# Optimization experiments

Hardware: AMD Instinct MI355X
Metric: run time of the kernel (lower is better)

## Reference

```python
import jax, jax.numpy as jnp
import numpy as np

B, S, I, H, L, O = 64, 512, 128, 1024, 3, 128


def _gru_cell(x, h, Wx, Wh, bh):
    # Wx: [3, H, in], Wh: [3, H, H], bh: [3, H]; gate order (z, r, g).
    # Matches: z = sig(W_xz x + W_hz h + b_z); r = sig(W_xr x + W_hr h + b_r);
    #          g = tanh(W_xg x + W_hg (r*h) + b_g); h' = z*h + (1-z)*g
    z = jax.nn.sigmoid(x @ Wx[0].T + h @ Wh[0].T + bh[0])
    r = jax.nn.sigmoid(x @ Wx[1].T + h @ Wh[1].T + bh[1])
    g = jnp.tanh(x @ Wx[2].T + (r * h) @ Wh[2].T + bh[2])
    return z * h + (1.0 - z) * g


def setup_inputs() -> dict:
    key = jax.random.key(0)
    ks = jax.random.split(key, 10)
    u = lambda k, shape, fan: jax.random.uniform(k, shape, jnp.float32, -1.0, 1.0) / np.float32(np.sqrt(fan))
    return {
        "x": jax.random.normal(ks[0], (B, S, I), jnp.float32),
        # layer 0 (input dim I)
        "Wx0": u(ks[1], (3, H, I), I),
        "Wh0": u(ks[2], (3, H, H), H),
        "bh0": u(ks[3], (3, H), H),
        # layers 1..L-1 (input dim H), stacked on leading axis
        "Wxr": u(ks[4], (L - 1, 3, H, H), H),
        "Whr": u(ks[5], (L - 1, 3, H, H), H),
        "bhr": u(ks[6], (L - 1, 3, H), H),
        # output projection
        "Wout": u(ks[7], (O, H), H),
        "bout": u(ks[8], (O,), H),
    }


def reference(x, Wx0, Wh0, bh0, Wxr, Whr, bhr, Wout, bout):
    batch = x.shape[0]
    n_rest = Wxr.shape[0]
    h_init = jnp.zeros((n_rest + 1, batch, H), x.dtype)  # [L, B, H]

    def step(hs, x_t):
        new = []
        h = _gru_cell(x_t, hs[0], Wx0, Wh0, bh0)
        new.append(h)
        inp = h
        for j in range(n_rest):  # small fixed layer count
            h = _gru_cell(inp, hs[j + 1], Wxr[j], Whr[j], bhr[j])
            new.append(h)
            inp = h
        y = inp @ Wout.T + bout
        return jnp.stack(new), y

    hs_final, ys = jax.lax.scan(step, h_init, jnp.swapaxes(x, 0, 1))
    layer_output = jnp.swapaxes(ys, 0, 1)        # (B, S, O)
    hidden_state = jnp.swapaxes(hs_final, 0, 1)  # (B, L, H)
    return layer_output, hidden_state
```

## Files before the change

### kernel.cpp

```cpp
#include <hip/hip_runtime.h>


namespace {
constexpr int kB = 64, kS = 512, kI = 128, kH = 1024, kO = 128;
constexpr int kTicks = kS + 3;
constexpr size_t kBSO = (size_t)kB * kS * kO;
constexpr int kTasksA = 792, kTasksB = 384;

__device__ float g_wxt0[3 * 128 * 1024];
__device__ float g_wht0[3 * 1024 * 1024];
__device__ float g_wxtr[6 * 1024 * 1024];
__device__ float g_whtr[6 * 1024 * 1024];
__device__ float g_woutT[1024 * 128];
__device__ float g_xT[512 * 128 * 64];
__device__ float g_hbuf[2 * 3 * 1024 * 64];
__device__ float g_zT[3 * 1024 * 64];
__device__ float g_rhT[3 * 1024 * 64];
__device__ float g_gxT[3 * 1024 * 64];
__device__ float g_partA[kTasksA * 4096];
__device__ float g_partB[kTasksB * 4096];
}


__global__ void zero_hbuf() {
  g_hbuf[blockIdx.x * 256 + threadIdx.x] = 0.f;
}

__global__ __launch_bounds__(256) void transpose_k(
    const float* __restrict__ in, int sel, int R, int C) {
  float* out;
  switch (sel) {
    case 0: out = g_wxt0; break;
    case 1: out = g_wht0; break;
    case 2: out = g_wxtr; break;
    case 3: out = g_whtr; break;
    case 4: out = g_woutT; break;
    default: out = g_xT; break;
  }
  const size_t mat = (size_t)R * C;
  in += blockIdx.z * mat;
  out += blockIdx.z * mat;
  __shared__ float t[32][33];
  const int c0 = blockIdx.x * 32, r0 = blockIdx.y * 32;
  const int tx = threadIdx.x & 31, ty = threadIdx.x >> 5;
  for (int i = ty; i < 32; i += 8) {
    const int r = r0 + i, c = c0 + tx;
    if (r < R && c < C) t[i][tx] = in[(size_t)r * C + c];
  }
  __syncthreads();
  for (int i = ty; i < 32; i += 8) {
    const int c = c0 + i, r = r0 + tx;
    if (c < C && r < R) out[(size_t)c * R + r] = t[tx][i];
  }
}

__device__ __forceinline__ void load_lds16(const float* g, float* l) {
  __builtin_amdgcn_global_load_lds(
      (const __attribute__((address_space(1))) void*)g,
      (__attribute__((address_space(3))) void*)l, 16, 0, 0);
}

__global__ __launch_bounds__(256, 2) void gemm_tasks(int phase, int tau) {
  const int id = blockIdx.x;
  const int par = tau & 1;
  const float* hb = g_hbuf + par * 196608;

  int l = 0, t_l = 0;
  const float* inp = nullptr; const float* w = nullptr;
  const float* inp2 = nullptr; const float* w2 = nullptr;
  int nk = 0, nk2 = 0, ldw = 1024;

  if (phase == 0) {
    if (id < 128) {
      const int gate = id >> 6, rem = id & 63;
      const int tile = rem >> 2, ks = rem & 3, n0 = tile * 64;
      t_l = tau;
      const float* wh = g_wht0 + (size_t)gate * 1048576;
      if (ks == 0) {
        inp = g_xT + (size_t)t_l * 8192; nk = 128;
        w = g_wxt0 + (size_t)gate * 131072 + n0;
        inp2 = hb; nk2 = 256; w2 = wh + n0;
      } else {
        const int k0 = ks * 256;
        inp = hb + k0 * 64; nk = 256;
        w = wh + (size_t)k0 * 1024 + n0;
      }
    } else if (id < 640) {
      const int q = id - 128;
      l = 1 + (q >> 8);
      const int qq = q & 255, gate = qq >> 7, rem = qq & 127;
      const int tile = rem >> 3, ks = rem & 7, n0 = tile * 64;
      t_l = tau - l;
      if (ks < 4) {
        const int k0 = ks * 256;
        inp = hb + (l - 1) * 65536 + k0 * 64; nk = 256;
        w = g_wxtr + (size_t)((l - 1) * 3 + gate) * 1048576 + (size_t)k0 * 1024 + n0;
      } else {
        const int k0 = (ks - 4) * 256;
        inp = hb + l * 65536 + k0 * 64; nk = 256;
        w = g_whtr + (size_t)((l - 1) * 3 + gate) * 1048576 + (size_t)k0 * 1024 + n0;
      }
    } else if (id < 656) {
      const int tile = id - 640;
      t_l = tau;
      inp = g_xT + (size_t)t_l * 8192; nk = 128;
      w = g_wxt0 + (size_t)2 * 131072 + tile * 64;
    } else if (id < 784) {
      const int q = id - 656;
      l = 1 + (q >> 6);
      const int qq = q & 63, tile = qq >> 2, ks = qq & 3;
      t_l = tau - l;
      const int k0 = ks * 256;
      inp = hb + (l - 1) * 65536 + k0 * 64; nk = 256;
      w = g_wxtr + (size_t)((l - 1) * 3 + 2) * 1048576 + (size_t)k0 * 1024 + tile * 64;
    } else {
      const int q = id - 784, tile = q >> 2, ks = q & 3;
      t_l = tau - 3;
      const int k0 = ks * 256;
      inp = hb + 2 * 65536 + k0 * 64; nk = 256;
      w = g_woutT + (size_t)k0 * 128 + tile * 64; ldw = 128;
    }
  } else {
    l = id >> 7;
    const int rem = id & 127, tile = rem >> 3, ks = rem & 7;
    t_l = tau - l;
    const int k0 = ks * 128;
    inp = g_rhT + l * 65536 + k0 * 64; nk = 128;
    w = ((l == 0) ? g_wht0 + (size_t)2 * 1048576
                  : g_whtr + (size_t)((l - 1) * 3 + 2) * 1048576) +
        (size_t)k0 * 1024 + tile * 64;
  }
  if (t_l < 0 || t_l >= kS) return;

  __shared__ float sI[64 * 64];
  __shared__ float sW[64 * 64];
  const int tid = threadIdx.x;
  const int tn = (tid & 15) * 4, tb = (tid >> 4) * 4;
  float acc[4][4] = {};

  for (int seg = 0; seg < 2; ++seg) {
    const float* ip; const float* wp; int kn;
    if (seg == 0) { ip = inp; wp = w; kn = nk; }
    else { if (!nk2) break; ip = inp2; wp = w2; kn = nk2; }
    for (int c0 = 0; c0 < kn; c0 += 64) {
#pragma unroll
      for (int u = 0; u < 4; ++u) {
        const int idx = tid + u * 256;
        load_lds16(ip + c0 * 64 + idx * 4, sI + idx * 4);
      }
#pragma unroll
      for (int u = 0; u < 4; ++u) {
        const int idx = tid + u * 256, k = idx >> 4, f = idx & 15;
        load_lds16(wp + (size_t)(c0 + k) * ldw + f * 4, sW + idx * 4);
      }
      __syncthreads();
#pragma unroll 8
      for (int k = 0; k < 64; ++k) {
        const float4 a = *(const float4*)(sI + k * 64 + tb);
        const float4 wv = *(const float4*)(sW + k * 64 + tn);
        acc[0][0] += wv.x * a.x; acc[0][1] += wv.x * a.y; acc[0][2] += wv.x * a.z; acc[0][3] += wv.x * a.w;
        acc[1][0] += wv.y * a.x; acc[1][1] += wv.y * a.y; acc[1][2] += wv.y * a.z; acc[1][3] += wv.y * a.w;
        acc[2][0] += wv.z * a.x; acc[2][1] += wv.z * a.y; acc[2][2] += wv.z * a.z; acc[2][3] += wv.z * a.w;
        acc[3][0] += wv.w * a.x; acc[3][1] += wv.w * a.y; acc[3][2] += wv.w * a.z; acc[3][3] += wv.w * a.w;
      }
      __syncthreads();
    }
  }

  float* po = ((phase == 0) ? g_partA : g_partB) + (size_t)id * 4096;
#pragma unroll
  for (int i = 0; i < 4; ++i) {
    float4 v = {acc[i][0], acc[i][1], acc[i][2], acc[i][3]};
    *(float4*)(po + (tn + i) * 64 + tb) = v;
  }
}

__global__ __launch_bounds__(256) void reduceA(
    int tau, const float* __restrict__ Bh0, const float* __restrict__ Bhr,
    const float* __restrict__ Bout, float* __restrict__ Out) {
  const int gid = blockIdx.x * 256 + threadIdx.x;
  const int b0 = (gid & 15) * 4, c = gid >> 4;
  const int par = tau & 1;
  if (c < 6144) {
    const int gate = (c >= 3072) ? 1 : 0;
    const int cc = c - gate * 3072;
    const int l = cc >> 10, n = cc & 1023;
    const int t_l = tau - l;
    if (t_l < 0 || t_l >= kS) return;
    const int tile = n >> 6, cl = n & 63;
    int base, nks;
    if (l == 0)      { base = gate * 64 + tile * 4;        nks = 4; }
    else if (l == 1) { base = 128 + gate * 128 + tile * 8; nks = 8; }
    else             { base = 384 + gate * 128 + tile * 8; nks = 8; }
    const float bias = (l == 0) ? Bh0[gate * 1024 + n] : Bhr[(l - 1) * 3072 + gate * 1024 + n];
    float s0 = bias, s1 = bias, s2 = bias, s3 = bias;
    for (int j = 0; j < nks; ++j) {
      const float4 p = *(const float4*)&g_partA[(size_t)(base + j) * 4096 + cl * 64 + b0];
      s0 += p.x; s1 += p.y; s2 += p.z; s3 += p.w;
    }
    const float v0 = 1.f / (1.f + expf(-s0)), v1 = 1.f / (1.f + expf(-s1));
    const float v2 = 1.f / (1.f + expf(-s2)), v3 = 1.f / (1.f + expf(-s3));
    const int off = l * 65536 + n * 64 + b0;
    if (gate == 0) {
      *(float4*)&g_zT[off] = make_float4(v0, v1, v2, v3);
    } else {
      const float4 h = *(const float4*)&g_hbuf[par * 196608 + off];
      *(float4*)&g_rhT[off] = make_float4(v0 * h.x, v1 * h.y, v2 * h.z, v3 * h.w);
    }
  } else if (c < 9216) {
    const int cc = c - 6144, l = cc >> 10, n = cc & 1023;
    const int t_l = tau - l;
    if (t_l < 0 || t_l >= kS) return;
    const int tile = n >> 6, cl = n & 63;
    int base, nks;
    if (l == 0)      { base = 640 + tile;     nks = 1; }
    else if (l == 1) { base = 656 + tile * 4; nks = 4; }
    else             { base = 720 + tile * 4; nks = 4; }
    const float bias = (l == 0) ? Bh0[2048 + n] : Bhr[(l - 1) * 3072 + 2048 + n];
    float s0 = bias, s1 = bias, s2 = bias, s3 = bias;
    for (int j = 0; j < nks; ++j) {
      const float4 p = *(const float4*)&g_partA[(size_t)(base + j) * 4096 + cl * 64 + b0];
      s0 += p.x; s1 += p.y; s2 += p.z; s3 += p.w;
    }
    *(float4*)&g_gxT[l * 65536 + n * 64 + b0] = make_float4(s0, s1, s2, s3);
  } else {
    const int o = c - 9216, ty = tau - 3;
    if (ty < 0 || ty >= kS) return;
    const int tile = o >> 6, cl = o & 63, base = 784 + tile * 4;
    const float bias = Bout[o];
    float s0 = bias, s1 = bias, s2 = bias, s3 = bias;
    for (int j = 0; j < 4; ++j) {
      const float4 p = *(const float4*)&g_partA[(size_t)(base + j) * 4096 + cl * 64 + b0];
      s0 += p.x; s1 += p.y; s2 += p.z; s3 += p.w;
    }
    Out[((size_t)(b0 + 0) * kS + ty) * kO + o] = s0;
    Out[((size_t)(b0 + 1) * kS + ty) * kO + o] = s1;
    Out[((size_t)(b0 + 2) * kS + ty) * kO + o] = s2;
    Out[((size_t)(b0 + 3) * kS + ty) * kO + o] = s3;
  }
}

__global__ __launch_bounds__(256) void reduceB(
    int tau, float* __restrict__ Out) {
  const int gid = blockIdx.x * 256 + threadIdx.x;
  const int b0 = (gid & 15) * 4, c = gid >> 4;
  const int l = c >> 10, n = c & 1023;
  const int t_l = tau - l;
  if (t_l < 0 || t_l >= kS) return;
  const int par = tau & 1;
  const int tile = n >> 6, cl = n & 63;
  const int base = (l * 16 + tile) * 8;
  const int off = l * 65536 + n * 64 + b0;
  float4 gs = *(const float4*)&g_gxT[off];
  for (int j = 0; j < 8; ++j) {
    const float4 p = *(const float4*)&g_partB[(size_t)(base + j) * 4096 + cl * 64 + b0];
    gs.x += p.x; gs.y += p.y; gs.z += p.z; gs.w += p.w;
  }
  const float g0 = tanhf(gs.x), g1 = tanhf(gs.y), g2 = tanhf(gs.z), g3 = tanhf(gs.w);
  const float4 z = *(const float4*)&g_zT[off];
  const float4 h = *(const float4*)&g_hbuf[par * 196608 + off];
  float4 hn;
  hn.x = z.x * h.x + (1.f - z.x) * g0;
  hn.y = z.y * h.y + (1.f - z.y) * g1;
  hn.z = z.z * h.z + (1.f - z.z) * g2;
  hn.w = z.w * h.w + (1.f - z.w) * g3;
  *(float4*)&g_hbuf[(1 - par) * 196608 + off] = hn;
  if (t_l == kS - 1) {
    Out[kBSO + ((size_t)(b0 + 0) * 3 + l) * 1024 + n] = hn.x;
    Out[kBSO + ((size_t)(b0 + 1) * 3 + l) * 1024 + n] = hn.y;
    Out[kBSO + ((size_t)(b0 + 2) * 3 + l) * 1024 + n] = hn.z;
    Out[kBSO + ((size_t)(b0 + 3) * 3 + l) * 1024 + n] = hn.w;
  }
}

extern "C" void kernel_launch(void* const* d_in, const int* in_sizes, int n_in,
                              void* d_out, int out_size, void* d_ws, size_t ws_size,
                              hipStream_t stream) {
  const float* X    = (const float*)d_in[0];
  const float* Wx0  = (const float*)d_in[1];
  const float* Wh0  = (const float*)d_in[2];
  const float* bh0  = (const float*)d_in[3];
  const float* Wxr  = (const float*)d_in[4];
  const float* Whr  = (const float*)d_in[5];
  const float* bhr  = (const float*)d_in[6];
  const float* Wout = (const float*)d_in[7];
  const float* bout = (const float*)d_in[8];
  (void)d_ws; (void)ws_size;

  if (n_in != 9 ||
      in_sizes[0] != 64 * 512 * 128 || in_sizes[1] != 3 * 1024 * 128 ||
      in_sizes[2] != 3 * 1024 * 1024 || in_sizes[3] != 3 * 1024 ||
      in_sizes[4] != 2 * 3 * 1024 * 1024 || in_sizes[5] != 2 * 3 * 1024 * 1024 ||
      in_sizes[6] != 2 * 3 * 1024 || in_sizes[7] != 128 * 1024 ||
      in_sizes[8] != 128 || out_size != 64 * 512 * 128 + 64 * 3 * 1024)
    return;

  float* out = (float*)d_out;

  hipLaunchKernelGGL(zero_hbuf, dim3(1536), dim3(256), 0, stream);
  hipLaunchKernelGGL(transpose_k, dim3(4, 32, 3),   dim3(256), 0, stream, Wx0,  0, 1024, 128);
  hipLaunchKernelGGL(transpose_k, dim3(32, 32, 3),  dim3(256), 0, stream, Wh0,  1, 1024, 1024);
  hipLaunchKernelGGL(transpose_k, dim3(32, 32, 6),  dim3(256), 0, stream, Wxr,  2, 1024, 1024);
  hipLaunchKernelGGL(transpose_k, dim3(32, 32, 6),  dim3(256), 0, stream, Whr,  3, 1024, 1024);
  hipLaunchKernelGGL(transpose_k, dim3(32, 4, 1),   dim3(256), 0, stream, Wout, 4, 128, 1024);
  hipLaunchKernelGGL(transpose_k, dim3(2048, 2, 1), dim3(256), 0, stream, X,    5, 64, 65536);

  for (int tau = 0; tau < kTicks; ++tau) {
    hipLaunchKernelGGL(gemm_tasks, dim3(kTasksA), dim3(256), 0, stream, 0, tau);
    hipLaunchKernelGGL(reduceA, dim3(584), dim3(256), 0, stream,
                       tau, bh0, bhr, bout, out);
    if (tau < kTicks - 1) {
      hipLaunchKernelGGL(gemm_tasks, dim3(kTasksB), dim3(256), 0, stream, 1, tau);
      hipLaunchKernelGGL(reduceB, dim3(192), dim3(256), 0, stream, tau, out);
    }
  }
}
```

Baseline: 26.47 ms.

## Widen GEMM task tiles to 128 columns with 512-thread blocks and deeper K splits

Each GEMM task now covers 128 output columns with 512-thread blocks and 512-deep K slices, where it used to cover 64 columns with 256-deep slices. This cuts the task counts (792→218, 384→96), the partial sums written and read by the reduce kernels, and repeated loads of the input activations. The x-projection and Wh segments for layer 0 are now split into separate tasks instead of being chained in one block. In exchange, far fewer blocks run on a GPU with many CUs (MI355X), and each block does longer serial K loops, so parallelism may drop.

Result: slower. 32.70 ms (+23.6%).

```diff
diff --git a/kernel.cpp b/kernel.cpp
--- a/kernel.cpp
+++ b/kernel.cpp
@@ -5,7 +5,7 @@
 constexpr int kB = 64, kS = 512, kI = 128, kH = 1024, kO = 128;
 constexpr int kTicks = kS + 3;
 constexpr size_t kBSO = (size_t)kB * kS * kO;
-constexpr int kTasksA = 792, kTasksB = 384;
+constexpr int kTasksA = 218, kTasksB = 96;
 
 __device__ float g_wxt0[3 * 128 * 1024];
 __device__ float g_wht0[3 * 1024 * 1024];
@@ -17,8 +17,8 @@
 __device__ float g_zT[3 * 1024 * 64];
 __device__ float g_rhT[3 * 1024 * 64];
 __device__ float g_gxT[3 * 1024 * 64];
-__device__ float g_partA[kTasksA * 4096];
-__device__ float g_partB[kTasksB * 4096];
+__device__ float g_partA[kTasksA * 8192];
+__device__ float g_partB[kTasksB * 8192];
 }
 
 
@@ -60,114 +60,100 @@
       (__attribute__((address_space(3))) void*)l, 16, 0, 0);
 }
 
-__global__ __launch_bounds__(256, 2) void gemm_tasks(int phase, int tau) {
+__global__ __launch_bounds__(512) void gemm_tasks(int phase, int tau) {
   const int id = blockIdx.x;
   const int par = tau & 1;
   const float* hb = g_hbuf + par * 196608;
 
-  int l = 0, t_l = 0;
+  int t_l = 0, nk = 512, ldw = 1024;
   const float* inp = nullptr; const float* w = nullptr;
-  const float* inp2 = nullptr; const float* w2 = nullptr;
-  int nk = 0, nk2 = 0, ldw = 1024;
 
   if (phase == 0) {
-    if (id < 128) {
-      const int gate = id >> 6, rem = id & 63;
-      const int tile = rem >> 2, ks = rem & 3, n0 = tile * 64;
+    if (id < 48) {
+      const int gate = id / 24, q = id % 24, ng = q / 3, ks = q % 3;
       t_l = tau;
-      const float* wh = g_wht0 + (size_t)gate * 1048576;
       if (ks == 0) {
         inp = g_xT + (size_t)t_l * 8192; nk = 128;
-        w = g_wxt0 + (size_t)gate * 131072 + n0;
-        inp2 = hb; nk2 = 256; w2 = wh + n0;
+        w = g_wxt0 + (size_t)gate * 131072 + ng * 128;
       } else {
-        const int k0 = ks * 256;
-        inp = hb + k0 * 64; nk = 256;
-        w = wh + (size_t)k0 * 1024 + n0;
+        const int k0 = (ks - 1) * 512;
+        inp = hb + k0 * 64;
+        w = g_wht0 + (size_t)gate * 1048576 + (size_t)k0 * 1024 + ng * 128;
       }
-    } else if (id < 640) {
-      const int q = id - 128;
-      l = 1 + (q >> 8);
-      const int qq = q & 255, gate = qq >> 7, rem = qq & 127;
-      const int tile = rem >> 3, ks = rem & 7, n0 = tile * 64;
+    } else if (id < 176) {
+      const int q = id - 48, l = 1 + (q >> 6);
+      const int q2 = q & 63, gate = q2 >> 5, q3 = q2 & 31, ng = q3 >> 2, ks = q3 & 3;
       t_l = tau - l;
-      if (ks < 4) {
-        const int k0 = ks * 256;
-        inp = hb + (l - 1) * 65536 + k0 * 64; nk = 256;
-        w = g_wxtr + (size_t)((l - 1) * 3 + gate) * 1048576 + (size_t)k0 * 1024 + n0;
+      if (ks < 2) {
+        const int k0 = ks * 512;
+        inp = hb + (l - 1) * 65536 + k0 * 64;
+        w = g_wxtr + (size_t)((l - 1) * 3 + gate) * 1048576 + (size_t)k0 * 1024 + ng * 128;
       } else {
-        const int k0 = (ks - 4) * 256;
-        inp = hb + l * 65536 + k0 * 64; nk = 256;
-        w = g_whtr + (size_t)((l - 1) * 3 + gate) * 1048576 + (size_t)k0 * 1024 + n0;
+        const int k0 = (ks - 2) * 512;
+        inp = hb + l * 65536 + k0 * 64;
+        w = g_whtr + (size_t)((l - 1) * 3 + gate) * 1048576 + (size_t)k0 * 1024 + ng * 128;
       }
-    } else if (id < 656) {
-      const int tile = id - 640;
+    } else if (id < 184) {
+      const int ng = id - 176;
       t_l = tau;
       inp = g_xT + (size_t)t_l * 8192; nk = 128;
-      w = g_wxt0 + (size_t)2 * 131072 + tile * 64;
-    } else if (id < 784) {
-      const int q = id - 656;
-      l = 1 + (q >> 6);
-      const int qq = q & 63, tile = qq >> 2, ks = qq & 3;
+      w = g_wxt0 + (size_t)2 * 131072 + ng * 128;
+    } else if (id < 216) {
+      const int q = id - 184, l = 1 + (q >> 4);
+      const int q2 = q & 15, ng = q2 >> 1, ks = q2 & 1;
       t_l = tau - l;
-      const int k0 = ks * 256;
-      inp = hb + (l - 1) * 65536 + k0 * 64; nk = 256;
-      w = g_wxtr + (size_t)((l - 1) * 3 + 2) * 1048576 + (size_t)k0 * 1024 + tile * 64;
+      const int k0 = ks * 512;
+      inp = hb + (l - 1) * 65536 + k0 * 64;
+      w = g_wxtr + (size_t)((l - 1) * 3 + 2) * 1048576 + (size_t)k0 * 1024 + ng * 128;
     } else {
-      const int q = id - 784, tile = q >> 2, ks = q & 3;
+      const int ks = id - 216;
       t_l = tau - 3;
-      const int k0 = ks * 256;
-      inp = hb + 2 * 65536 + k0 * 64; nk = 256;
-      w = g_woutT + (size_t)k0 * 128 + tile * 64; ldw = 128;
+      const int k0 = ks * 512;
+      inp = hb + 2 * 65536 + k0 * 64;
+      w = g_woutT + (size_t)k0 * 128; ldw = 128;
     }
   } else {
-    l = id >> 7;
-    const int rem = id & 127, tile = rem >> 3, ks = rem & 7;
+    const int l = id >> 5, q = id & 31, ng = q >> 2, ks = q & 3;
     t_l = tau - l;
-    const int k0 = ks * 128;
-    inp = g_rhT + l * 65536 + k0 * 64; nk = 128;
+    const int k0 = ks * 256;
+    inp = g_rhT + l * 65536 + k0 * 64; nk = 256;
     w = ((l == 0) ? g_wht0 + (size_t)2 * 1048576
                   : g_whtr + (size_t)((l - 1) * 3 + 2) * 1048576) +
-        (size_t)k0 * 1024 + tile * 64;
+        (size_t)k0 * 1024 + ng * 128;
   }
   if (t_l < 0 || t_l >= kS) return;
 
   __shared__ float sI[64 * 64];
-  __shared__ float sW[64 * 64];
+  __shared__ float sW[64 * 128];
   const int tid = threadIdx.x;
-  const int tn = (tid & 15) * 4, tb = (tid >> 4) * 4;
+  const int tn = (tid & 31) * 4, tb = (tid >> 5) * 4;
   float acc[4][4] = {};
 
-  for (int seg = 0; seg < 2; ++seg) {
-    const float* ip; const float* wp; int kn;
-    if (seg == 0) { ip = inp; wp = w; kn = nk; }
-    else { if (!nk2) break; ip = inp2; wp = w2; kn = nk2; }
-    for (int c0 = 0; c0 < kn; c0 += 64) {
+  for (int c0 = 0; c0 < nk; c0 += 64) {
 #pragma unroll
-      for (int u = 0; u < 4; ++u) {
-        const int idx = tid + u * 256;
-        load_lds16(ip + c0 * 64 + idx * 4, sI + idx * 4);
-      }
+    for (int u = 0; u < 2; ++u) {
+      const int idx = tid + u * 512;
+      load_lds16(inp + c0 * 64 + idx * 4, sI + idx * 4);
+    }
 #pragma unroll
-      for (int u = 0; u < 4; ++u) {
-        const int idx = tid + u * 256, k = idx >> 4, f = idx & 15;
-        load_lds16(wp + (size_t)(c0 + k) * ldw + f * 4, sW + idx * 4);
-      }
-      __syncthreads();
+    for (int u = 0; u < 4; ++u) {
+      const int idx = tid + u * 512, k = idx >> 5, f = idx & 31;
+      load_lds16(w + (size_t)(c0 + k) * ldw + f * 4, sW + idx * 4);
+    }
+    __syncthreads();
 #pragma unroll 8
-      for (int k = 0; k < 64; ++k) {
-        const float4 a = *(const float4*)(sI + k * 64 + tb);
-        const float4 wv = *(const float4*)(sW + k * 64 + tn);
-        acc[0][0] += wv.x * a.x; acc[0][1] += wv.x * a.y; acc[0][2] += wv.x * a.z; acc[0][3] += wv.x * a.w;
-        acc[1][0] += wv.y * a.x; acc[1][1] += wv.y * a.y; acc[1][2] += wv.y * a.z; acc[1][3] += wv.y * a.w;
-        acc[2][0] += wv.z * a.x; acc[2][1] += wv.z * a.y; acc[2][2] += wv.z * a.z; acc[2][3] += wv.z * a.w;
-        acc[3][0] += wv.w * a.x; acc[3][1] += wv.w * a.y; acc[3][2] += wv.w * a.z; acc[3][3] += wv.w * a.w;
-      }
-      __syncthreads();
-    }
-  }
-
-  float* po = ((phase == 0) ? g_partA : g_partB) + (size_t)id * 4096;
+    for (int k = 0; k < 64; ++k) {
+      const float4 a = *(const float4*)(sI + k * 64 + tb);
+      const float4 wv = *(const float4*)(sW + k * 128 + tn);
+      acc[0][0] += wv.x * a.x; acc[0][1] += wv.x * a.y; acc[0][2] += wv.x * a.z; acc[0][3] += wv.x * a.w;
+      acc[1][0] += wv.y * a.x; acc[1][1] += wv.y * a.y; acc[1][2] += wv.y * a.z; acc[1][3] += wv.y * a.w;
+      acc[2][0] += wv.z * a.x; acc[2][1] += wv.z * a.y; acc[2][2] += wv.z * a.z; acc[2][3] += wv.z * a.w;
+      acc[3][0] += wv.w * a.x; acc[3][1] += wv.w * a.y; acc[3][2] += wv.w * a.z; acc[3][3] += wv.w * a.w;
+    }
+    __syncthreads();
+  }
+
+  float* po = ((phase == 0) ? g_partA : g_partB) + (size_t)id * 8192;
 #pragma unroll
   for (int i = 0; i < 4; ++i) {
     float4 v = {acc[i][0], acc[i][1], acc[i][2], acc[i][3]};
@@ -187,15 +173,14 @@
     const int l = cc >> 10, n = cc & 1023;
     const int t_l = tau - l;
     if (t_l < 0 || t_l >= kS) return;
-    const int tile = n >> 6, cl = n & 63;
+    const int ng = n >> 7, cl = n & 127;
     int base, nks;
-    if (l == 0)      { base = gate * 64 + tile * 4;        nks = 4; }
-    else if (l == 1) { base = 128 + gate * 128 + tile * 8; nks = 8; }
-    else             { base = 384 + gate * 128 + tile * 8; nks = 8; }
+    if (l == 0) { base = gate * 24 + ng * 3;                  nks = 3; }
+    else        { base = 48 + (l - 1) * 64 + gate * 32 + ng * 4; nks = 4; }
     const float bias = (l == 0) ? Bh0[gate * 1024 + n] : Bhr[(l - 1) * 3072 + gate * 1024 + n];
     float s0 = bias, s1 = bias, s2 = bias, s3 = bias;
     for (int j = 0; j < nks; ++j) {
-      const float4 p = *(const float4*)&g_partA[(size_t)(base + j) * 4096 + cl * 64 + b0];
+      const float4 p = *(const float4*)&g_partA[(size_t)(base + j) * 8192 + cl * 64 + b0];
       s0 += p.x; s1 += p.y; s2 += p.z; s3 += p.w;
     }
     const float v0 = 1.f / (1.f + expf(-s0)), v1 = 1.f / (1.f + expf(-s1));
@@ -211,26 +196,24 @@
     const int cc = c - 6144, l = cc >> 10, n = cc & 1023;
     const int t_l = tau - l;
     if (t_l < 0 || t_l >= kS) return;
-    const int tile = n >> 6, cl = n & 63;
+    const int ng = n >> 7, cl = n & 127;
     int base, nks;
-    if (l == 0)      { base = 640 + tile;     nks = 1; }
-    else if (l == 1) { base = 656 + tile * 4; nks = 4; }
-    else             { base = 720 + tile * 4; nks = 4; }
+    if (l == 0) { base = 176 + ng;                 nks = 1; }
+    else        { base = 184 + (l - 1) * 16 + ng * 2; nks = 2; }
     const float bias = (l == 0) ? Bh0[2048 + n] : Bhr[(l - 1) * 3072 + 2048 + n];
     float s0 = bias, s1 = bias, s2 = bias, s3 = bias;
     for (int j = 0; j < nks; ++j) {
-      const float4 p = *(const float4*)&g_partA[(size_t)(base + j) * 4096 + cl * 64 + b0];
+      const float4 p = *(const float4*)&g_partA[(size_t)(base + j) * 8192 + cl * 64 + b0];
       s0 += p.x; s1 += p.y; s2 += p.z; s3 += p.w;
     }
     *(float4*)&g_gxT[l * 65536 + n * 64 + b0] = make_float4(s0, s1, s2, s3);
   } else {
     const int o = c - 9216, ty = tau - 3;
     if (ty < 0 || ty >= kS) return;
-    const int tile = o >> 6, cl = o & 63, base = 784 + tile * 4;
     const float bias = Bout[o];
     float s0 = bias, s1 = bias, s2 = bias, s3 = bias;
-    for (int j = 0; j < 4; ++j) {
-      const float4 p = *(const float4*)&g_partA[(size_t)(base + j) * 4096 + cl * 64 + b0];
+    for (int j = 0; j < 2; ++j) {
+      const float4 p = *(const float4*)&g_partA[(size_t)(216 + j) * 8192 + o * 64 + b0];
       s0 += p.x; s1 += p.y; s2 += p.z; s3 += p.w;
     }
     Out[((size_t)(b0 + 0) * kS + ty) * kO + o] = s0;
@@ -248,12 +231,12 @@
   const int t_l = tau - l;
   if (t_l < 0 || t_l >= kS) return;
   const int par = tau & 1;
-  const int tile = n >> 6, cl = n & 63;
-  const int base = (l * 16 + tile) * 8;
+  const int ng = n >> 7, cl = n & 127;
+  const int base = l * 32 + ng * 4;
   const int off = l * 65536 + n * 64 + b0;
   float4 gs = *(const float4*)&g_gxT[off];
-  for (int j = 0; j < 8; ++j) {
-    const float4 p = *(const float4*)&g_partB[(size_t)(base + j) * 4096 + cl * 64 + b0];
+  for (int j = 0; j < 4; ++j) {
+    const float4 p = *(const float4*)&g_partB[(size_t)(base + j) * 8192 + cl * 64 + b0];
     gs.x += p.x; gs.y += p.y; gs.z += p.z; gs.w += p.w;
   }
   const float g0 = tanhf(gs.x), g1 = tanhf(gs.y), g2 = tanhf(gs.z), g3 = tanhf(gs.w);
@@ -306,11 +289,11 @@
   hipLaunchKernelGGL(transpose_k, dim3(2048, 2, 1), dim3(256), 0, stream, X,    5, 64, 65536);
 
   for (int tau = 0; tau < kTicks; ++tau) {
-    hipLaunchKernelGGL(gemm_tasks, dim3(kTasksA), dim3(256), 0, stream, 0, tau);
+    hipLaunchKernelGGL(gemm_tasks, dim3(kTasksA), dim3(512), 0, stream, 0, tau);
     hipLaunchKernelGGL(reduceA, dim3(584), dim3(256), 0, stream,
                        tau, bh0, bhr, bout, out);
     if (tau < kTicks - 1) {
-      hipLaunchKernelGGL(gemm_tasks, dim3(kTasksB), dim3(256), 0, stream, 1, tau);
+      hipLaunchKernelGGL(gemm_tasks, dim3(kTasksB), dim3(512), 0, stream, 1, tau);
       hipLaunchKernelGGL(reduceB, dim3(192), dim3(256), 0, stream, tau, out);
     }
   }
```
